# Kernel optimization log

Measured on AMD Instinct MI355X. Metric: run time of the kernel, lower is better.

Reference implementation:

```python
import jax, jax.numpy as jnp
import numpy as np

# Module constants (from init_kwargs)
BETA = 0.1
DX = 10.0 / 2048  # X / N
DT = 0.002        # CFL: 0.75 * dx / max|f'|
BATCH = 128
N = 2048
STEPNUM = 256


def flux(u):
    # f_real with is_real=True:
    # f = 0.5*u*(3 - u^2) + beta/12 * u^2 * (3/4 - 2u + 3/2 u^2 - 1/4 u^4)
    u2 = u * u
    return 0.5 * u * (3.0 - u2) + (BETA / 12.0) * u2 * (
        0.75 - 2.0 * u + 1.5 * u2 - 0.25 * u2 * u2)


def flux_prime(u):
    # Closed-form elementwise derivative of flux (what torch autograd.grad computes
    # per grid point, since f is elementwise in u):
    # f'(u) = 1.5*(1 - u^2) + beta/12 * (1.5u - 6u^2 + 6u^3 - 1.5u^5)
    u2 = u * u
    u3 = u2 * u
    return 1.5 * (1.0 - u2) + (BETA / 12.0) * (
        1.5 * u - 6.0 * u2 + 6.0 * u3 - 1.5 * u2 * u3)


def setup_inputs() -> dict:
    key = jax.random.key(0)
    init = jax.random.uniform(key, (BATCH, N), dtype=jnp.float32)  # u in [0,1]
    return {"init": init, "stepnum": STEPNUM}


def reference(init, stepnum):
    dt_over_dx = jnp.float32(DT / DX)

    def step(u, _):
        f = flux(u)                              # [B, N]
        a = jnp.abs(flux_prime(u))               # [B, N]
        # Local Lax-Friedrichs (Rusanov) wave speed: max over the 2-point stencil
        alpha = jnp.maximum(a[:, :-1], a[:, 1:])  # [B, N-1]
        f_half = 0.5 * (f[:, :-1] + f[:, 1:]) - 0.5 * alpha * (u[:, 1:] - u[:, :-1])
        # Interior update for j = 1..N-2
        u_inner = u[:, 1:-1] - dt_over_dx * (f_half[:, 1:] - f_half[:, :-1])
        # Outflow boundaries: u[0] = u[1], u[N-1] = u[N-2] (with u[1], u[N-2] updated)
        u_new = jnp.concatenate([u_inner[:, :1], u_inner, u_inner[:, -1:]], axis=1)
        return u_new, u_new

    _, traj = jax.lax.scan(step, init, None, length=stepnum - 1)  # [S-1, B, N]
    return jnp.concatenate([init[None], traj], axis=0)           # [S, B, N]
```

## Files before the change

### kernel.cpp

```cpp
#include <hip/hip_runtime.h>

#define BATCH 128
#define NCELL 2048
#define OWN 512
#define HALO 256
#define WIDTH 1024
#define NTHREADS 256

typedef float f32x4 __attribute__((ext_vector_type(4)));

__device__ __forceinline__ float flux_h(float u, float u2) {
    float h = fmaf(u2, -0.0020833333333333333f, 0.0125f);
    h = fmaf(u, h, -0.5166666666666667f);
    h = fmaf(u, h, 0.00625f);
    h = fmaf(u, h, 1.5f);
    return u * h;
}
__device__ __forceinline__ float aprime_h(float u, float u2) {
    float h = fmaf(u2, -0.0125f, 0.05f);
    h = fmaf(u, h, -1.55f);
    h = fmaf(u, h, 0.0125f);
    h = fmaf(u, h, 1.5f);
    return fabsf(h);
}

__global__ __launch_bounds__(NTHREADS)
void VariantCoeLinear1d_kernel(const float* __restrict__ init,
                               const int* __restrict__ stepnum_p,
                               float* __restrict__ out) {
    __shared__ float ubuf[2][WIDTH];

    const int b = blockIdx.x;
    const int row = b >> 2;
    const int q = b & 3;
    const int t = threadIdx.x;
    const int S = *stepnum_p;
    const float c = 0.4096f;

    const int ownedLo = q * OWN;
    const int ownedHi = ownedLo + OWN - 1;
    const int base = ownedLo - HALO;
    const int li = t << 2;
    const int g0 = base + li;

    const float* rin = init + (size_t)row * NCELL;
    float u0, u1, u2, u3;
    if (g0 >= 0 && g0 + 3 < NCELL) {
        float4 v = *(const float4*)(rin + g0);
        u0 = v.x; u1 = v.y; u2 = v.z; u3 = v.w;
    } else {
        u0 = rin[min(max(g0 + 0, 0), NCELL - 1)];
        u1 = rin[min(max(g0 + 1, 0), NCELL - 1)];
        u2 = rin[min(max(g0 + 2, 0), NCELL - 1)];
        u3 = rin[min(max(g0 + 3, 0), NCELL - 1)];
    }

    const bool owned = (t >= HALO / 4) && (t < (HALO + OWN) / 4);
    float* op = out + (size_t)row * NCELL + g0;
    if (owned) {
        __builtin_nontemporal_store((f32x4){u0, u1, u2, u3}, (f32x4*)op);
    }

    int cur = 0;
    for (int s = 1; s < S; ++s) {
        float* ub = ubuf[cur];
        *(float4*)&ub[li] = make_float4(u0, u1, u2, u3);
        asm volatile("s_waitcnt lgkmcnt(0)\n\ts_barrier" ::: "memory");

        const int rem = (S - 1) - s;
        const int lo = max(ownedLo - rem, 0);
        const int hi = min(ownedHi + rem, NCELL - 1);
        op += (size_t)BATCH * NCELL;

        if (g0 + 3 >= lo && g0 <= hi) {
            const float ulm = ub[max(li - 1, 0)];
            const float ulp = ub[min(li + 4, WIDTH - 1)];
            float ul[6] = {ulm, u0, u1, u2, u3, ulp};
            float f[6], a[6];
#pragma unroll
            for (int j = 0; j < 6; ++j) {
                const float uu = ul[j], uu2 = uu * uu;
                f[j] = flux_h(uu, uu2);
                a[j] = aprime_h(uu, uu2);
            }
            float fh[5];
#pragma unroll
            for (int j = 0; j < 5; ++j) {
                fh[j] = 0.5f * (f[j] + f[j + 1])
                      - 0.5f * fmaxf(a[j], a[j + 1]) * (ul[j + 1] - ul[j]);
            }
            float un[4];
#pragma unroll
            for (int i = 0; i < 4; ++i) {
                un[i] = ul[i + 1] - c * (fh[i + 1] - fh[i]);
                const int g = g0 + i;
                un[i] = (g >= lo && g <= hi) ? un[i] : ul[i + 1];
            }
            if (g0 == 0) un[0] = un[1];
            if (g0 + 3 == NCELL - 1) un[3] = un[2];
            u0 = un[0]; u1 = un[1]; u2 = un[2]; u3 = un[3];

            if (owned) {
                __builtin_nontemporal_store((f32x4){u0, u1, u2, u3}, (f32x4*)op);
            }
        }
        cur ^= 1;
    }
}

extern "C" void kernel_launch(void* const* d_in, const int* in_sizes, int n_in,
                              void* d_out, int out_size, void* d_ws, size_t ws_size,
                              hipStream_t stream) {
    const float* init = (const float*)d_in[0];
    const int* stepnum = (const int*)d_in[1];
    float* out = (float*)d_out;

    dim3 grid(BATCH * 4);
    dim3 block(NTHREADS);
    VariantCoeLinear1d_kernel<<<grid, block, 0, stream>>>(init, stepnum, out);
}
```

Baseline: 335.0 us.

## Fuse four time steps per barrier using a per-thread register halo

Each thread now loads a 4-cell halo on each side from shared memory and advances four time steps in registers, with the valid region shrinking by one cell per substep. The goal is to cut shared-memory exchanges and barriers per step by a factor of four. In exchange, every thread does redundant flux evaluations on halo cells and holds more registers, and shared memory gains guard cells filled with edge values.

```diff
diff --git a/kernel.cpp b/kernel.cpp
--- a/kernel.cpp
+++ b/kernel.cpp
@@ -6,6 +6,7 @@
 #define HALO 256
 #define WIDTH 1024
 #define NTHREADS 256
+#define GUARD 4
 
 typedef float f32x4 __attribute__((ext_vector_type(4)));
 
@@ -24,11 +25,44 @@
     return fabsf(h);
 }
 
+template <int J>
+__device__ __forceinline__ void substep(float (&w)[12], int g0m4, int lo,
+                                        int hi, float c) {
+    float f[12], a[12];
+#pragma unroll
+    for (int i = J; i <= 11 - J; ++i) {
+        const float uu = w[i], uu2 = uu * uu;
+        f[i] = flux_h(uu, uu2);
+        a[i] = aprime_h(uu, uu2);
+    }
+    float fh[11];
+#pragma unroll
+    for (int i = J; i <= 10 - J; ++i) {
+        fh[i] = 0.5f * (f[i] + f[i + 1])
+              - 0.5f * fmaxf(a[i], a[i + 1]) * (w[i + 1] - w[i]);
+    }
+    float un[12];
+#pragma unroll
+    for (int i = J + 1; i <= 10 - J; ++i) {
+        const int g = g0m4 + i;
+        const float v = w[i] - c * (fh[i] - fh[i - 1]);
+        un[i] = (g >= lo && g <= hi) ? v : w[i];
+    }
+#pragma unroll
+    for (int i = J + 1; i <= 10 - J; ++i) {
+        const int g = g0m4 + i;
+        float v = un[i];
+        if (i <= 9 - J)  v = (g == 0) ? un[i + 1] : v;
+        if (i >= J + 2)  v = (g == NCELL - 1) ? un[i - 1] : v;
+        w[i] = v;
+    }
+}
+
 __global__ __launch_bounds__(NTHREADS)
 void VariantCoeLinear1d_kernel(const float* __restrict__ init,
                                const int* __restrict__ stepnum_p,
                                float* __restrict__ out) {
-    __shared__ float ubuf[2][WIDTH];
+    __shared__ float ubuf[2][WIDTH + 2 * GUARD];
 
     const int b = blockIdx.x;
     const int row = b >> 2;
@@ -42,66 +76,79 @@
     const int base = ownedLo - HALO;
     const int li = t << 2;
     const int g0 = base + li;
+    const int g0m4 = g0 - 4;
 
     const float* rin = init + (size_t)row * NCELL;
-    float u0, u1, u2, u3;
+    float w[12];
     if (g0 >= 0 && g0 + 3 < NCELL) {
         float4 v = *(const float4*)(rin + g0);
-        u0 = v.x; u1 = v.y; u2 = v.z; u3 = v.w;
+        w[4] = v.x; w[5] = v.y; w[6] = v.z; w[7] = v.w;
     } else {
-        u0 = rin[min(max(g0 + 0, 0), NCELL - 1)];
-        u1 = rin[min(max(g0 + 1, 0), NCELL - 1)];
-        u2 = rin[min(max(g0 + 2, 0), NCELL - 1)];
-        u3 = rin[min(max(g0 + 3, 0), NCELL - 1)];
+        w[4] = rin[min(max(g0 + 0, 0), NCELL - 1)];
+        w[5] = rin[min(max(g0 + 1, 0), NCELL - 1)];
+        w[6] = rin[min(max(g0 + 2, 0), NCELL - 1)];
+        w[7] = rin[min(max(g0 + 3, 0), NCELL - 1)];
     }
 
     const bool owned = (t >= HALO / 4) && (t < (HALO + OWN) / 4);
+    const size_t stride = (size_t)BATCH * NCELL;
     float* op = out + (size_t)row * NCELL + g0;
     if (owned) {
-        __builtin_nontemporal_store((f32x4){u0, u1, u2, u3}, (f32x4*)op);
+        __builtin_nontemporal_store((f32x4){w[4], w[5], w[6], w[7]},
+                                    (f32x4*)op);
     }
 
     int cur = 0;
-    for (int s = 1; s < S; ++s) {
+    for (int s = 1; s < S; s += 4) {
         float* ub = ubuf[cur];
-        *(float4*)&ub[li] = make_float4(u0, u1, u2, u3);
+        *(float4*)&ub[li + GUARD] = make_float4(w[4], w[5], w[6], w[7]);
+        if (t == 0)
+            *(float4*)&ub[0] = make_float4(w[4], w[4], w[4], w[4]);
+        if (t == NTHREADS - 1)
+            *(float4*)&ub[WIDTH + GUARD] = make_float4(w[7], w[7], w[7], w[7]);
         asm volatile("s_waitcnt lgkmcnt(0)\n\ts_barrier" ::: "memory");
 
-        const int rem = (S - 1) - s;
-        const int lo = max(ownedLo - rem, 0);
-        const int hi = min(ownedHi + rem, NCELL - 1);
-        op += (size_t)BATCH * NCELL;
+        const int rem0 = (S - 1) - s;
+        const int lo0 = max(ownedLo - rem0, 0);
+        const int hi0 = min(ownedHi + rem0, NCELL - 1);
 
-        if (g0 + 3 >= lo && g0 <= hi) {
-            const float ulm = ub[max(li - 1, 0)];
-            const float ulp = ub[min(li + 4, WIDTH - 1)];
-            float ul[6] = {ulm, u0, u1, u2, u3, ulp};
-            float f[6], a[6];
-#pragma unroll
-            for (int j = 0; j < 6; ++j) {
-                const float uu = ul[j], uu2 = uu * uu;
-                f[j] = flux_h(uu, uu2);
-                a[j] = aprime_h(uu, uu2);
-            }
-            float fh[5];
-#pragma unroll
-            for (int j = 0; j < 5; ++j) {
-                fh[j] = 0.5f * (f[j] + f[j + 1])
-                      - 0.5f * fmaxf(a[j], a[j + 1]) * (ul[j + 1] - ul[j]);
-            }
-            float un[4];
-#pragma unroll
-            for (int i = 0; i < 4; ++i) {
-                un[i] = ul[i + 1] - c * (fh[i + 1] - fh[i]);
-                const int g = g0 + i;
-                un[i] = (g >= lo && g <= hi) ? un[i] : ul[i + 1];
-            }
-            if (g0 == 0) un[0] = un[1];
-            if (g0 + 3 == NCELL - 1) un[3] = un[2];
-            u0 = un[0]; u1 = un[1]; u2 = un[2]; u3 = un[3];
+        if (g0 + 7 >= lo0 && g0m4 <= hi0) {
+            const float4 hl = *(const float4*)&ub[li];
+            const float4 hr = *(const float4*)&ub[li + GUARD + 4];
+            w[0] = hl.x; w[1] = hl.y; w[2]  = hl.z; w[3]  = hl.w;
+            w[8] = hr.x; w[9] = hr.y; w[10] = hr.z; w[11] = hr.w;
 
-            if (owned) {
-                __builtin_nontemporal_store((f32x4){u0, u1, u2, u3}, (f32x4*)op);
+            substep<0>(w, g0m4, lo0, hi0, c);
+            op += stride;
+            if (owned)
+                __builtin_nontemporal_store((f32x4){w[4], w[5], w[6], w[7]},
+                                            (f32x4*)op);
+            if (s + 1 < S) {
+                const int rem = rem0 - 1;
+                substep<1>(w, g0m4, max(ownedLo - rem, 0),
+                           min(ownedHi + rem, NCELL - 1), c);
+                op += stride;
+                if (owned)
+                    __builtin_nontemporal_store(
+                        (f32x4){w[4], w[5], w[6], w[7]}, (f32x4*)op);
+                if (s + 2 < S) {
+                    const int rem2 = rem0 - 2;
+                    substep<2>(w, g0m4, max(ownedLo - rem2, 0),
+                               min(ownedHi + rem2, NCELL - 1), c);
+                    op += stride;
+                    if (owned)
+                        __builtin_nontemporal_store(
+                            (f32x4){w[4], w[5], w[6], w[7]}, (f32x4*)op);
+                    if (s + 3 < S) {
+                        const int rem3 = rem0 - 3;
+                        substep<3>(w, g0m4, max(ownedLo - rem3, 0),
+                                   min(ownedHi + rem3, NCELL - 1), c);
+                        op += stride;
+                        if (owned)
+                            __builtin_nontemporal_store(
+                                (f32x4){w[4], w[5], w[6], w[7]}, (f32x4*)op);
+                    }
+                }
             }
         }
         cur ^= 1;
```

New measurement: 378.2 us. +12.9%, slower.

## Split time stepping into two launches with a smaller halo

Applied to the files above, without the earlier changes.

The 255 time steps are split into two kernel launches of 128 steps each. The second launch restarts from the step-128 state already written to the output. Because each launch covers fewer steps, the trapezoidal halo shrinks from 256 to 128 cells, cutting block width from 1024 to 768 and threads from 256 to 192, which removes redundant halo computation and reduces barrier cost. It also adds a branch-free fast path for fully interior quads, at the cost of an extra launch and a round-trip of one time slice through global memory.

```diff
diff --git a/kernel.cpp b/kernel.cpp
--- a/kernel.cpp
+++ b/kernel.cpp
@@ -3,9 +3,10 @@
 #define BATCH 128
 #define NCELL 2048
 #define OWN 512
-#define HALO 256
-#define WIDTH 1024
-#define NTHREADS 256
+#define HALO 128
+#define WIDTH 768
+#define NTHREADS 192
+#define CHUNK 128
 
 typedef float f32x4 __attribute__((ext_vector_type(4)));
 
@@ -16,18 +17,19 @@
     h = fmaf(u, h, 1.5f);
     return u * h;
 }
-__device__ __forceinline__ float aprime_h(float u, float u2) {
+__device__ __forceinline__ float fp_h(float u, float u2) {
     float h = fmaf(u2, -0.0125f, 0.05f);
     h = fmaf(u, h, -1.55f);
     h = fmaf(u, h, 0.0125f);
     h = fmaf(u, h, 1.5f);
-    return fabsf(h);
+    return h;
 }
 
 __global__ __launch_bounds__(NTHREADS)
-void VariantCoeLinear1d_kernel(const float* __restrict__ init,
+void VariantCoeLinear1d_kernel(const float* __restrict__ src,
                                const int* __restrict__ stepnum_p,
-                               float* __restrict__ out) {
+                               float* __restrict__ out,
+                               int s_begin, int store_init) {
     __shared__ float ubuf[2][WIDTH];
 
     const int b = blockIdx.x;
@@ -35,6 +37,7 @@
     const int q = b & 3;
     const int t = threadIdx.x;
     const int S = *stepnum_p;
+    const int s_last = min(s_begin + (CHUNK - 1), S - 1);
     const float c = 0.4096f;
 
     const int ownedLo = q * OWN;
@@ -43,7 +46,7 @@
     const int li = t << 2;
     const int g0 = base + li;
 
-    const float* rin = init + (size_t)row * NCELL;
+    const float* rin = src + (size_t)row * NCELL;
     float u0, u1, u2, u3;
     if (g0 >= 0 && g0 + 3 < NCELL) {
         float4 v = *(const float4*)(rin + g0);
@@ -56,21 +59,24 @@
     }
 
     const bool owned = (t >= HALO / 4) && (t < (HALO + OWN) / 4);
-    float* op = out + (size_t)row * NCELL + g0;
-    if (owned) {
+    const bool isL = (g0 == 0);
+    const bool isR = (g0 + 3 == NCELL - 1);
+    const size_t stride = (size_t)BATCH * NCELL;
+    float* op = out + ((size_t)(s_begin - 1) * BATCH + row) * NCELL + g0;
+    if (store_init && owned) {
         __builtin_nontemporal_store((f32x4){u0, u1, u2, u3}, (f32x4*)op);
     }
 
     int cur = 0;
-    for (int s = 1; s < S; ++s) {
+    for (int s = s_begin; s <= s_last; ++s) {
         float* ub = ubuf[cur];
         *(float4*)&ub[li] = make_float4(u0, u1, u2, u3);
         asm volatile("s_waitcnt lgkmcnt(0)\n\ts_barrier" ::: "memory");
 
-        const int rem = (S - 1) - s;
+        const int rem = s_last - s;
         const int lo = max(ownedLo - rem, 0);
         const int hi = min(ownedHi + rem, NCELL - 1);
-        op += (size_t)BATCH * NCELL;
+        op += stride;
 
         if (g0 + 3 >= lo && g0 <= hi) {
             const float ulm = ub[max(li - 1, 0)];
@@ -81,27 +87,35 @@
             for (int j = 0; j < 6; ++j) {
                 const float uu = ul[j], uu2 = uu * uu;
                 f[j] = flux_h(uu, uu2);
-                a[j] = aprime_h(uu, uu2);
+                a[j] = fp_h(uu, uu2);
             }
             float fh[5];
 #pragma unroll
             for (int j = 0; j < 5; ++j) {
                 fh[j] = 0.5f * (f[j] + f[j + 1])
-                      - 0.5f * fmaxf(a[j], a[j + 1]) * (ul[j + 1] - ul[j]);
+                      - 0.5f * fmaxf(fabsf(a[j]), fabsf(a[j + 1]))
+                             * (ul[j + 1] - ul[j]);
             }
-            float un[4];
+            if (g0 >= lo && g0 + 3 <= hi && !isL && !isR) {
+                u0 = ul[1] - c * (fh[1] - fh[0]);
+                u1 = ul[2] - c * (fh[2] - fh[1]);
+                u2 = ul[3] - c * (fh[3] - fh[2]);
+                u3 = ul[4] - c * (fh[4] - fh[3]);
+            } else {
+                float un[4];
 #pragma unroll
-            for (int i = 0; i < 4; ++i) {
-                un[i] = ul[i + 1] - c * (fh[i + 1] - fh[i]);
-                const int g = g0 + i;
-                un[i] = (g >= lo && g <= hi) ? un[i] : ul[i + 1];
+                for (int i = 0; i < 4; ++i) {
+                    un[i] = ul[i + 1] - c * (fh[i + 1] - fh[i]);
+                    const int g = g0 + i;
+                    un[i] = (g >= lo && g <= hi) ? un[i] : ul[i + 1];
+                }
+                if (isL) un[0] = un[1];
+                if (isR) un[3] = un[2];
+                u0 = un[0]; u1 = un[1]; u2 = un[2]; u3 = un[3];
             }
-            if (g0 == 0) un[0] = un[1];
-            if (g0 + 3 == NCELL - 1) un[3] = un[2];
-            u0 = un[0]; u1 = un[1]; u2 = un[2]; u3 = un[3];
-
             if (owned) {
-                __builtin_nontemporal_store((f32x4){u0, u1, u2, u3}, (f32x4*)op);
+                __builtin_nontemporal_store((f32x4){u0, u1, u2, u3},
+                                            (f32x4*)op);
             }
         }
         cur ^= 1;
@@ -114,8 +128,12 @@
     const float* init = (const float*)d_in[0];
     const int* stepnum = (const int*)d_in[1];
     float* out = (float*)d_out;
+    const size_t stride = (size_t)BATCH * NCELL;
 
     dim3 grid(BATCH * 4);
     dim3 block(NTHREADS);
-    VariantCoeLinear1d_kernel<<<grid, block, 0, stream>>>(init, stepnum, out);
+    VariantCoeLinear1d_kernel<<<grid, block, 0, stream>>>(
+        init, stepnum, out, 1, 1);
+    VariantCoeLinear1d_kernel<<<grid, block, 0, stream>>>(
+        out + (size_t)CHUNK * stride, stepnum, out, CHUNK + 1, 0);
 }
```

New measurement: 377.2 us. 12.6% more time.
